# Optimization experiments

Hardware: AMD Instinct MI355X
Metric: run time of the kernel (lower is better)

## Reference

```python
import jax, jax.numpy as jnp
import numpy as np

B, S, D, F, E, K, R, H = 4, 1024, 1024, 512, 8, 2, 64, 256
TEMP = 1.0          # step=0 -> 0.5+0.5*cos(0)=1.0, clamp(min=0.1) -> 1.0
BW, EW, ZW = 0.3, 0.1, 1e-4


def fq(t):
    """Per-tensor symmetric int8 fake-quant with straight-through estimator."""
    s = jnp.maximum(jnp.max(jnp.abs(t)) / 127.0, 1e-8)
    q = jnp.clip(jnp.round(t / s), -128, 127) * s
    return t + jax.lax.stop_gradient(q - t)


def lora_lin(h, W, A, Bm):
    # base weight is frozen (requires_grad=False) and fake-quantized
    y = h @ fq(jax.lax.stop_gradient(W)).T + (h @ Bm.T) @ A.T
    return fq(y)


def ffn(h, w1, a1, b1, w2, a2, b2, w3, a3, b3):
    # use_swiglu=True path: gate = sigmoid(w3(x)); out = w2(w1(x)*gate); dropout=eval identity
    gate = jax.nn.sigmoid(lora_lin(h, w3, a3, b3))
    out = lora_lin(lora_lin(h, w1, a1, b1) * gate, w2, a2, b2)
    return fq(out)


def setup_inputs() -> dict:
    key = jax.random.key(0)
    k = jax.random.split(key, 32)
    n = lambda i, shp: jax.random.normal(k[i], shp, dtype=jnp.float32) * 0.02
    return {
        "x": jax.random.normal(k[0], (B, S, D), dtype=jnp.float32),
        "scorer_w": n(1, (E, D)), "scorer_b": jnp.zeros((E,), jnp.float32),
        "p1_w": n(2, (H, D)), "p1_b": jnp.zeros((H,), jnp.float32),
        "p2_w": n(3, (E, H)), "p2_b": jnp.zeros((E,), jnp.float32),
        "ew1_w": n(4, (E, F, D)), "ew1_a": n(5, (E, F, R)), "ew1_b": n(6, (E, R, D)),
        "ew2_w": n(7, (E, D, F)), "ew2_a": n(8, (E, D, R)), "ew2_b": n(9, (E, R, F)),
        "ew3_w": n(10, (E, F, D)), "ew3_a": n(11, (E, F, R)), "ew3_b": n(12, (E, R, D)),
        "s1_w": n(13, (F, D)), "s1_a": n(14, (F, R)), "s1_b": n(15, (R, D)),
        "s2_w": n(16, (D, F)), "s2_a": n(17, (D, R)), "s2_b": n(18, (R, F)),
        "s3_w": n(19, (F, D)), "s3_a": n(20, (F, R)), "s3_b": n(21, (R, D)),
    }


def reference(x, scorer_w, scorer_b, p1_w, p1_b, p2_w, p2_b,
              ew1_w, ew1_a, ew1_b, ew2_w, ew2_a, ew2_b, ew3_w, ew3_a, ew3_b,
              s1_w, s1_a, s1_b, s2_w, s2_a, s2_b, s3_w, s3_a, s3_b):
    xf = x.reshape(-1, D)                                           # [T, D]
    # --- router (per-token) ---
    base = (xf @ scorer_w.T + scorer_b) / TEMP                      # [T, E]
    policy = jax.nn.softmax(jax.nn.relu(xf @ p1_w.T + p1_b) @ p2_w.T + p2_b, axis=-1)
    scores = jax.nn.softmax((base + policy) * 0.5, axis=-1)         # fp32 softmax
    entropy = -(scores * jnp.log(scores + 1e-6)).sum(-1).mean()
    z_loss = ZW * (jax.nn.logsumexp(base, axis=-1) ** 2).mean()
    weights, indices = jax.lax.top_k(scores, K)                     # [T, K]
    weights = weights * TEMP
    cw = (jax.nn.one_hot(indices, E, dtype=weights.dtype) * weights[..., None]).sum(1)  # [T, E]
    usage = cw.sum(0)                                               # [E]
    uf = usage / (usage.mean() + 1e-6)
    balance_loss = BW * jnp.var(uf, ddof=1) - EW * entropy + z_loss
    # --- expert dispatch: dense masked combine (faithful to weighted scatter-add) ---
    eout = jax.vmap(lambda w1, a1, b1, w2, a2, b2, w3, a3, b3:
                    ffn(xf, w1, a1, b1, w2, a2, b2, w3, a3, b3))(
        ew1_w, ew1_a, ew1_b, ew2_w, ew2_a, ew2_b, ew3_w, ew3_a, ew3_b)  # [E, T, D]
    y = jnp.einsum('te,etd->td', cw, eout)                          # weighted combine
    z = ffn(xf, s1_w, s1_a, s1_b, s2_w, s2_a, s2_b, s3_w, s3_a, s3_b)
    out = (y + z).reshape(x.shape)
    return (out, usage, balance_loss, jnp.float32(0.0), jnp.float32(0.0))
```

## Files before the change

### kernel.cpp

```cpp
#include <hip/hip_runtime.h>

#define TTOK 4096
#define DDIM 1024
#define FDIM 512
#define NEXP 8
#define HDIM 256
#define RLORA 64
#define CROWS 14336

using u16 = unsigned short;
using f4v = __attribute__((ext_vector_type(4))) float;
using bfrag = __attribute__((ext_vector_type(8))) short;
using u16x8 = __attribute__((ext_vector_type(8))) unsigned short;

static __device__ __forceinline__ float bf2f(u16 u) {
  union { unsigned int u; float f; } x; x.u = ((unsigned int)u) << 16; return x.f;
}
static __device__ __forceinline__ u16 f2bf(float f) {
  union { float f; unsigned int u; } x; x.f = f;
  unsigned int r = (x.u + 0x7fffu + ((x.u >> 16) & 1u)) >> 16;
  return (u16)r;
}
static __device__ __forceinline__ float fq1(float t, float s) {
  float q = rintf(t / s);
  q = fminf(fmaxf(q, -128.f), 127.f);
  return q * s;
}

struct GemmGArgs {
  const u16* A; const u16* B; u16* C;
  const int* tokmap; const int2* blkmap; const int* nbrow;
};

#define STAGE1(d, kt, h, l) \
  __builtin_amdgcn_global_load_lds( \
    (const __attribute__((address_space(1))) void*)(gs[(h)*2+(l)] + (size_t)(kt)*64), \
    (__attribute__((address_space(3))) void*)&lds[(d)*32768 + (h)*8192 + (tid + (l)*512)*8], \
    16, 0, 0)

template <int MODE>
__global__ __launch_bounds__(512, 2) void gemm256g(GemmGArgs g) {
  const int br = blockIdx.x;
  if (br >= g.nbrow[0]) return;
  const int2 bm = g.blkmap[br];
  const int e = bm.x;
  const int m0 = bm.y;
  const int n0 = blockIdx.y * 256;
  const int tid = threadIdx.x;
  const int lane = tid & 63;
  const int wave = tid >> 6;
  const int wr = wave >> 2;
  const int wc = wave & 3;

  constexpr int K = MODE ? 1024 : 512;
  const u16* Bp = g.B + (size_t)e * (MODE ? 1048576 : 524288);

  __shared__ u16 lds[65536];

  const u16* gs[8];
#pragma unroll
  for (int h = 0; h < 4; h++)
#pragma unroll
    for (int l = 0; l < 2; l++) {
      const int slot = tid + l * 512;
      const int row = slot >> 3, p = slot & 7;
      const int glog = p ^ (row & 7);
      const u16* basep;
      if (h < 2) {
        const int grow = m0 + h * 128 + row;
        const int t = MODE ? g.tokmap[grow] : grow;
        basep = g.A + (size_t)t * K;
      } else {
        basep = Bp + (size_t)(n0 + (h - 2) * 128 + row) * K;
      }
      gs[h * 2 + l] = basep + glog * 8;
    }

  f4v acc[8][4];
#pragma unroll
  for (int i = 0; i < 8; i++)
#pragma unroll
    for (int j = 0; j < 4; j++) acc[i][j] = (f4v){0.f, 0.f, 0.f, 0.f};

  const int q = lane >> 4;
  const int lx = lane & 7;
  const int l15 = lane & 15;

#pragma unroll
  for (int h = 0; h < 4; h++) { STAGE1(0, 0, h, 0); STAGE1(0, 0, h, 1); }
  __syncthreads();

  constexpr int nt = K >> 6;
  for (int kt = 0; kt < nt; ++kt) {
    const int d = kt & 1;
    const int dn = d ^ 1;
    const bool more = (kt + 1 < nt);
#pragma unroll
    for (int kk = 0; kk < 2; ++kk) {
      if (more) {
        if (kk == 0) { STAGE1(dn, kt + 1, 0, 0); STAGE1(dn, kt + 1, 0, 1);
                       STAGE1(dn, kt + 1, 1, 0); STAGE1(dn, kt + 1, 1, 1); }
        else         { STAGE1(dn, kt + 1, 2, 0); STAGE1(dn, kt + 1, 2, 1);
                       STAGE1(dn, kt + 1, 3, 0); STAGE1(dn, kt + 1, 3, 1); }
      }
      bfrag afr[8], bfr[4];
      const int pa = ((kk * 4 + q) ^ lx) << 3;
      const int abase = d * 32768 + wr * 8192 + l15 * 64 + pa;
#pragma unroll
      for (int mi = 0; mi < 8; mi++) afr[mi] = *(const bfrag*)&lds[abase + mi * 1024];
      const int bbase = d * 32768 + (2 + (wc >> 1)) * 8192 + (((wc & 1) << 6) + l15) * 64 + pa;
#pragma unroll
      for (int ni = 0; ni < 4; ni++) bfr[ni] = *(const bfrag*)&lds[bbase + ni * 1024];
      __builtin_amdgcn_s_setprio(1);
#pragma unroll
      for (int mi = 0; mi < 8; mi++)
#pragma unroll
        for (int ni = 0; ni < 4; ni++)
          acc[mi][ni] = __builtin_amdgcn_mfma_f32_16x16x32_bf16(afr[mi], bfr[ni], acc[mi][ni], 0, 0, 0);
      __builtin_amdgcn_s_setprio(0);
    }
    __syncthreads();
  }

  const int crow0 = m0 + wr * 128 + q * 4;

  if (MODE == 1) {
    float* xlds = (float*)lds;
    const int lrow0 = wr * 128 + q * 4;
    if (wc >= 2) {
      const int lc = (wc - 2) * 64 + l15;
#pragma unroll
      for (int mi = 0; mi < 8; mi++)
#pragma unroll
        for (int ni = 0; ni < 4; ni++)
#pragma unroll
          for (int r = 0; r < 4; r++)
            xlds[(lrow0 + mi * 16 + r) * 128 + lc + ni * 16] = acc[mi][ni][r];
    }
    __syncthreads();
    if (wc < 2) {
      const int lc = wc * 64 + l15;
      const int fbase = (n0 >> 1) + lc;
#pragma unroll
      for (int mi = 0; mi < 8; mi++)
#pragma unroll
        for (int r = 0; r < 4; r++) {
          const int rowg = crow0 + mi * 16 + r;
          const int lr = lrow0 + mi * 16 + r;
#pragma unroll
          for (int ni = 0; ni < 4; ni++) {
            float y1 = acc[mi][ni][r];
            float y3 = xlds[lr * 128 + lc + ni * 16];
            float h = y1 / (1.f + __expf(-y3));
            g.C[(size_t)rowg * FDIM + fbase + ni * 16] = f2bf(h);
          }
        }
    }
  } else {
    const int ccol0 = n0 + wc * 64 + l15;
#pragma unroll
    for (int mi = 0; mi < 8; mi++)
#pragma unroll
      for (int ni = 0; ni < 4; ni++) {
        const int col = ccol0 + ni * 16;
#pragma unroll
        for (int r = 0; r < 4; r++)
          g.C[(size_t)(crow0 + mi * 16 + r) * 1024 + col] = f2bf(acc[mi][ni][r]);
      }
  }
}

struct FoldArgs {
  const u16* A0; const u16* B0;
  const u16* Wb;
  u16* C13; u16* C2e;
  const float* sW;
};

__global__ __launch_bounds__(256) void gemm_fold(FoldArgs g) {
  const int z = blockIdx.z;
  const bool is13 = z < 18;
  const int bx = blockIdx.x, by = blockIdx.y;
  if (is13 ? (bx >= 4) : (by >= 4)) return;
  const int N = is13 ? 1024 : 512;
  const int K = 64;
  const u16* Ap = is13 ? g.A0 + (size_t)z * 32768 : g.A0 + 589824 + (size_t)(z - 18) * 65536;
  const u16* Bp = is13 ? g.B0 + (size_t)z * 65536 : g.B0 + 1179648 + (size_t)(z - 18) * 32768;
  const u16* Wf = g.Wb + (size_t)z * 524288;
  u16* Cb; int flag;
  if (is13) {
    const int slot = (z >= 16) ? 8 : (z & 7);
    Cb = g.C13 + (size_t)slot * 1048576;
    flag = (z >= 8 && z < 16) || z == 17 ? 2 : 1;
  } else {
    Cb = g.C2e + (size_t)(z - 18) * 524288;
    flag = 0;
  }
  const float sw = fmaxf(g.sW[z] / 127.f, 1e-8f);

  const int tid = threadIdx.x;
  const int lane = tid & 63;
  const int wave = tid >> 6;
  const int wr = wave >> 1, wc = wave & 1;
  const int m0 = bx * 128, n0 = by * 128;

  __shared__ u16 As[128 * 32];
  __shared__ u16 Bs[128 * 32];
  __shared__ u16 stage[128 * 136];

  const int ldrow = tid >> 2;
  const int swzcol = (((tid & 3) ^ ((tid >> 3) & 3)) << 3);
  const u16* ga = Ap + (size_t)(m0 + ldrow) * K + swzcol;
  const u16* gb = Bp + (size_t)(n0 + ldrow) * K + swzcol;
  const size_t rowstep = (size_t)64 * K;

  f4v acc[4][4];
#pragma unroll
  for (int i = 0; i < 4; i++)
#pragma unroll
    for (int j = 0; j < 4; j++) acc[i][j] = (f4v){0.f, 0.f, 0.f, 0.f};

  const int rbase = lane & 15;
  const int q = lane >> 4;
  const int pg = (q ^ ((rbase >> 1) & 3)) << 3;
  const int arow = (wr << 6) + rbase;
  const int brow = (wc << 6) + rbase;

  for (int kt = 0; kt < K; kt += 32) {
    __builtin_amdgcn_global_load_lds((const __attribute__((address_space(1))) void*)(ga),
        (__attribute__((address_space(3))) void*)&As[tid * 8], 16, 0, 0);
    __builtin_amdgcn_global_load_lds((const __attribute__((address_space(1))) void*)(ga + rowstep),
        (__attribute__((address_space(3))) void*)&As[(256 + tid) * 8], 16, 0, 0);
    __builtin_amdgcn_global_load_lds((const __attribute__((address_space(1))) void*)(gb),
        (__attribute__((address_space(3))) void*)&Bs[tid * 8], 16, 0, 0);
    __builtin_amdgcn_global_load_lds((const __attribute__((address_space(1))) void*)(gb + rowstep),
        (__attribute__((address_space(3))) void*)&Bs[(256 + tid) * 8], 16, 0, 0);
    ga += 32; gb += 32;
    __syncthreads();
    bfrag af[4], bf[4];
#pragma unroll
    for (int mi = 0; mi < 4; mi++)
      af[mi] = *(const bfrag*)&As[(arow + mi * 16) * 32 + pg];
#pragma unroll
    for (int ni = 0; ni < 4; ni++)
      bf[ni] = *(const bfrag*)&Bs[(brow + ni * 16) * 32 + pg];
#pragma unroll
    for (int mi = 0; mi < 4; mi++)
#pragma unroll
      for (int ni = 0; ni < 4; ni++)
        acc[mi][ni] = __builtin_amdgcn_mfma_f32_16x16x32_bf16(af[mi], bf[ni], acc[mi][ni], 0, 0, 0);
    __syncthreads();
  }

  const int lrow0 = (wr << 6) + ((lane >> 4) << 2);
  const int lcol0 = (wc << 6) + (lane & 15);
#pragma unroll
  for (int mi = 0; mi < 4; mi++)
#pragma unroll
    for (int ni = 0; ni < 4; ni++) {
      const int n = lcol0 + ni * 16;
#pragma unroll
      for (int r = 0; r < 4; r++)
        stage[(lrow0 + mi * 16 + r) * 136 + n] = f2bf(acc[mi][ni][r]);
    }
  __syncthreads();

  const int dm0 = flag ? (((m0 >> 7) << 8) + (flag == 2 ? 128 : 0)) : m0;
#pragma unroll
  for (int j = 0; j < 8; j++) {
    const int s = j * 256 + tid;
    const int lr = s >> 4;
    const int n8 = (s & 15) << 3;
    const u16x8 wv = *(const u16x8*)&Wf[(size_t)(m0 + lr) * N + n0 + n8];
    const bfrag sv = *(const bfrag*)&stage[lr * 136 + n8];
    u16x8 o;
#pragma unroll
    for (int k = 0; k < 8; k++)
      o[k] = f2bf(fq1(bf2f(wv[k]), sw) + bf2f((u16)sv[k]));
    *(u16x8*)&Cb[(size_t)(dm0 + lr) * N + n0 + n8] = o;
  }
}

struct Gemm64Args { const u16* A; const u16* B; u16* Cb; int M, N, K; const float* bias; };
__global__ __launch_bounds__(256) void gemm64(Gemm64Args g) {
  const int tid = threadIdx.x;
  const int lane = tid & 63;
  const int wave = tid >> 6;
  const int wr = wave >> 1, wc = wave & 1;
  const int m0 = blockIdx.x * 64, n0 = blockIdx.y * 64;
  const int K = g.K, N = g.N;

  __shared__ u16 As[64 * 32];
  __shared__ u16 Bs[64 * 32];

  const int ldrow = tid >> 2;
  const int swzcol = (((tid & 3) ^ ((tid >> 3) & 3)) << 3);
  const u16* ga = g.A + (size_t)(m0 + ldrow) * K + swzcol;
  const u16* gb = g.B + (size_t)(n0 + ldrow) * K + swzcol;

  f4v acc[2][2];
#pragma unroll
  for (int i = 0; i < 2; i++)
#pragma unroll
    for (int j = 0; j < 2; j++) acc[i][j] = (f4v){0.f, 0.f, 0.f, 0.f};

  const int rbase = lane & 15;
  const int q = lane >> 4;
  const int pg = (q ^ ((rbase >> 1) & 3)) << 3;
  const int arow = (wr << 5) + rbase;
  const int brow = (wc << 5) + rbase;

  for (int kt = 0; kt < K; kt += 32) {
    __builtin_amdgcn_global_load_lds((const __attribute__((address_space(1))) void*)(ga),
        (__attribute__((address_space(3))) void*)&As[tid * 8], 16, 0, 0);
    __builtin_amdgcn_global_load_lds((const __attribute__((address_space(1))) void*)(gb),
        (__attribute__((address_space(3))) void*)&Bs[tid * 8], 16, 0, 0);
    ga += 32; gb += 32;
    __syncthreads();
    bfrag af[2], bf[2];
#pragma unroll
    for (int mi = 0; mi < 2; mi++)
      af[mi] = *(const bfrag*)&As[(arow + mi * 16) * 32 + pg];
#pragma unroll
    for (int ni = 0; ni < 2; ni++)
      bf[ni] = *(const bfrag*)&Bs[(brow + ni * 16) * 32 + pg];
#pragma unroll
    for (int mi = 0; mi < 2; mi++)
#pragma unroll
      for (int ni = 0; ni < 2; ni++)
        acc[mi][ni] = __builtin_amdgcn_mfma_f32_16x16x32_bf16(af[mi], bf[ni], acc[mi][ni], 0, 0, 0);
    __syncthreads();
  }

  const int crow0 = m0 + (wr << 5) + ((lane >> 4) << 2);
  const int ccol0 = n0 + (wc << 5) + (lane & 15);
#pragma unroll
  for (int mi = 0; mi < 2; mi++)
#pragma unroll
    for (int ni = 0; ni < 2; ni++) {
      const int n = ccol0 + ni * 16;
      const float b = g.bias[n];
#pragma unroll
      for (int r = 0; r < 4; r++) {
        float v = fmaxf(acc[mi][ni][r] + b, 0.f);
        g.Cb[(size_t)(crow0 + mi * 16 + r) * N + n] = f2bf(v);
      }
    }
}

struct AmaxCArgs { const float* W[27]; u16* Wraw; float* amax; };
__global__ __launch_bounds__(256) void amax_convw(AmaxCArgs a) {
  const int t = blockIdx.y;
  const float4* src = (const float4*)a.W[t];
  ushort4* dst = (ushort4*)(a.Wraw + (size_t)t * 524288);
  float lmax = 0.f;
  for (int i = blockIdx.x * 256 + threadIdx.x; i < 131072; i += gridDim.x * 256) {
    float4 v = src[i];
    ushort4 o; o.x = f2bf(v.x); o.y = f2bf(v.y); o.z = f2bf(v.z); o.w = f2bf(v.w);
    dst[i] = o;
    lmax = fmaxf(lmax, fmaxf(fmaxf(fabsf(v.x), fabsf(v.y)), fmaxf(fabsf(v.z), fabsf(v.w))));
  }
#pragma unroll
  for (int off = 32; off > 0; off >>= 1) lmax = fmaxf(lmax, __shfl_xor(lmax, off));
  __shared__ float wm[4];
  if ((threadIdx.x & 63) == 0) wm[threadIdx.x >> 6] = lmax;
  __syncthreads();
  if (threadIdx.x == 0) {
    float m = fmaxf(fmaxf(wm[0], wm[1]), fmaxf(wm[2], wm[3]));
    atomicMax((unsigned int*)&a.amax[t], __float_as_uint(m));
  }
}

struct ConvArgs {
  const float* xf; u16* xfb;
  const float* p1w; u16* p1wb;
  const float* Asrc[27]; u16* Adst;
  const float* Bsrc[27]; u16* Bdst;
};
__global__ __launch_bounds__(256) void convert_kernel(ConvArgs a) {
  const int g0 = blockIdx.x * 256 + threadIdx.x;
  const int stride = gridDim.x * 256;
  if (blockIdx.y == 0) {
    for (int i = g0; i < 1048576; i += stride) {
      float4 v = ((const float4*)a.xf)[i];
      ushort4 o; o.x = f2bf(v.x); o.y = f2bf(v.y); o.z = f2bf(v.z); o.w = f2bf(v.w);
      ((ushort4*)a.xfb)[i] = o;
    }
  } else if (blockIdx.y == 1) {
    for (int i = g0; i < 65536; i += stride) {
      float4 v = ((const float4*)a.p1w)[i];
      ushort4 o; o.x = f2bf(v.x); o.y = f2bf(v.y); o.z = f2bf(v.z); o.w = f2bf(v.w);
      ((ushort4*)a.p1wb)[i] = o;
    }
  } else if (blockIdx.y == 2) {
    for (int i = g0; i < 1179648; i += stride) {
      int t, off;
      if (i < 589824) { t = i >> 15; off = i & 32767; }
      else { int j = i - 589824; t = 18 + (j >> 16); off = j & 65535; }
      a.Adst[i] = f2bf(a.Asrc[t][off]);
    }
  } else {
    for (int i = g0; i < 1474560; i += stride) {
      int t, src;
      if (i < 1179648) { t = i >> 16; int off = i & 65535; src = (off & 63) * 1024 + (off >> 6); }
      else { int j = i - 1179648; t = 18 + (j >> 15); int off = j & 32767; src = (off & 63) * 512 + (off >> 6); }
      a.Bdst[i] = f2bf(a.Bsrc[t][src]);
    }
  }
}

struct RouterArgs {
  const float* xf; const u16* ph;
  const float* sw; const float* sb;
  const float* p2w; const float* p2b;
  float* base; float* pol;
};
__global__ __launch_bounds__(256) void router_small(RouterArgs a) {
  __shared__ float sw[8][1024];
  __shared__ float p2[8][256];
  const int tid = threadIdx.x;
  {
    const float4* s0 = (const float4*)a.sw;
    float4* d0 = (float4*)&sw[0][0];
    for (int i = tid; i < 2048; i += 256) d0[i] = s0[i];
    const float4* s1 = (const float4*)a.p2w;
    float4* d1 = (float4*)&p2[0][0];
    for (int i = tid; i < 512; i += 256) d1[i] = s1[i];
  }
  __syncthreads();
  const int tl = tid >> 4, s = tid & 15;
  const int token = blockIdx.x * 16 + tl;
  float acc[8] = {0,0,0,0,0,0,0,0}, pacc[8] = {0,0,0,0,0,0,0,0};
  const float4* xrow = (const float4*)(a.xf + (size_t)token * 1024);
  for (int i = 0; i < 16; i++) {
    const int d4 = i * 16 + s;
    float4 xv = xrow[d4];
#pragma unroll
    for (int e = 0; e < 8; e++) {
      float4 wv = ((const float4*)&sw[e][0])[d4];
      acc[e] += xv.x * wv.x + xv.y * wv.y + xv.z * wv.z + xv.w * wv.w;
    }
  }
  const u16* phrow = a.ph + (size_t)token * 256;
  for (int i = 0; i < 16; i++) {
    const int h = i * 16 + s;
    float pv = bf2f(phrow[h]);
#pragma unroll
    for (int e = 0; e < 8; e++) pacc[e] += pv * p2[e][h];
  }
#pragma unroll
  for (int off = 8; off > 0; off >>= 1)
#pragma unroll
    for (int e = 0; e < 8; e++) {
      acc[e] += __shfl_xor(acc[e], off);
      pacc[e] += __shfl_xor(pacc[e], off);
    }
  if (s == 0) {
#pragma unroll
    for (int e = 0; e < 8; e++) {
      a.base[token * 8 + e] = acc[e] + a.sb[e];
      a.pol[token * 8 + e] = pacc[e] + a.p2b[e];
    }
  }
}

struct FinArgs {
  const float* base; const float* pol;
  float* partials;
  int* idx2; float2* wb; int* cnt;
};
__global__ __launch_bounds__(256) void router_topk(FinArgs a) {
  const int tid = threadIdx.x;
  const int lane = tid & 63, wv = tid >> 6;
  const int token = blockIdx.x * 256 + tid;
  float b[8], p[8];
#pragma unroll
  for (int e = 0; e < 8; e++) { b[e] = a.base[token * 8 + e]; p[e] = a.pol[token * 8 + e]; }
  float pm = p[0];
#pragma unroll
  for (int e = 1; e < 8; e++) pm = fmaxf(pm, p[e]);
  float pe[8], psum = 0.f;
#pragma unroll
  for (int e = 0; e < 8; e++) { pe[e] = expf(p[e] - pm); psum += pe[e]; }
  const float pinv = 1.f / psum;
  float sl[8];
#pragma unroll
  for (int e = 0; e < 8; e++) sl[e] = (b[e] + pe[e] * pinv) * 0.5f;
  float sm = sl[0];
#pragma unroll
  for (int e = 1; e < 8; e++) sm = fmaxf(sm, sl[e]);
  float sc[8], ssum = 0.f;
#pragma unroll
  for (int e = 0; e < 8; e++) { sc[e] = expf(sl[e] - sm); ssum += sc[e]; }
  const float sinv = 1.f / ssum;
  float ent = 0.f;
#pragma unroll
  for (int e = 0; e < 8; e++) { float v = sc[e] * sinv; sc[e] = v; ent -= v * logf(v + 1e-6f); }
  float bm = b[0];
#pragma unroll
  for (int e = 1; e < 8; e++) bm = fmaxf(bm, b[e]);
  float zs = 0.f;
#pragma unroll
  for (int e = 0; e < 8; e++) zs += expf(b[e] - bm);
  const float lse = logf(zs) + bm;
  const float zt = lse * lse;
  float m1 = -1e30f, m2 = -1e30f; int i1 = 0, i2 = 0;
#pragma unroll
  for (int e = 0; e < 8; e++) {
    float v = sc[e];
    if (v > m1) { m2 = m1; i2 = i1; m1 = v; i1 = e; }
    else if (v > m2) { m2 = v; i2 = e; }
  }
  a.idx2[token] = i1 | (i2 << 8);
  a.wb[token] = make_float2(m1, m2);

  __shared__ int hist[8];
  if (tid < 8) hist[tid] = 0;
  __syncthreads();
  atomicAdd(&hist[i1], 1);
  atomicAdd(&hist[i2], 1);
  __syncthreads();
  if (tid < 8) atomicAdd(&a.cnt[tid], hist[tid]);

  float vals[10];
  vals[0] = ent; vals[1] = zt;
#pragma unroll
  for (int e = 0; e < 8; e++) vals[2 + e] = 0.f;
  vals[2 + i1] = m1; vals[2 + i2] = m2;
#pragma unroll
  for (int v = 0; v < 10; v++)
#pragma unroll
    for (int off = 32; off > 0; off >>= 1) vals[v] += __shfl_down(vals[v], off);
  __shared__ float wred[4][10];
  if (lane == 0)
#pragma unroll
    for (int v = 0; v < 10; v++) wred[wv][v] = vals[v];
  __syncthreads();
  if (tid < 10)
    a.partials[blockIdx.x * 10 + tid] = wred[0][tid] + wred[1][tid] + wred[2][tid] + wred[3][tid];
}

__global__ void setup_finalize(const int* cnt, int* off, int2* blkmap, int* nbrow, int* tokmap,
                               const float* partials, float* tail) {
  if (threadIdx.x == 0) {
    int o = 0, nb = 16;
    for (int i = 0; i < 16; i++) blkmap[i] = make_int2(8, i * 256);
    for (int e = 0; e < 8; e++) {
      off[e] = o;
      const int nbe = (cnt[e] + 255) >> 8;
      for (int i = 0; i < nbe; i++) blkmap[nb++] = make_int2(e, 4096 + o + i * 256);
      o += nbe << 8;
    }
    nbrow[0] = nb;
  } else if (threadIdx.x == 64) {
    float ent = 0.f, z = 0.f, us[8] = {0,0,0,0,0,0,0,0};
    for (int i = 0; i < 16; i++) {
      ent += partials[i * 10 + 0];
      z += partials[i * 10 + 1];
      for (int e = 0; e < 8; e++) us[e] += partials[i * 10 + 2 + e];
    }
    float tot = 0.f;
    for (int e = 0; e < 8; e++) tot += us[e];
    const float meanu = tot / 8.f;
    float uf[8], mu = 0.f;
    for (int e = 0; e < 8; e++) { uf[e] = us[e] / (meanu + 1e-6f); mu += uf[e]; }
    mu /= 8.f;
    float var = 0.f;
    for (int e = 0; e < 8; e++) { float d = uf[e] - mu; var += d * d; }
    var /= 7.f;
    const float bl = 0.3f * var - 0.1f * (ent / 4096.f) + 1e-4f * (z / 4096.f);
    for (int e = 0; e < 8; e++) tail[e] = us[e];
    tail[8] = bl; tail[9] = 0.f; tail[10] = 0.f;
  }
  for (int t = threadIdx.x; t < 4096; t += blockDim.x) tokmap[t] = t;
  for (int t = 4096 + threadIdx.x; t < CROWS; t += blockDim.x) tokmap[t] = 0;
}

__global__ __launch_bounds__(256) void compact_lists(const int* idx2, const int* off,
                                                     int* tokmap, int* posb) {
  const int e = blockIdx.x;
  const int tid = threadIdx.x;
  const int lane = tid & 63, wv = tid >> 6;
  __shared__ int wtot[4];
  __shared__ int carry;
  if (tid == 0) carry = 0;
  __syncthreads();
  const int base = 4096 + off[e];
  for (int c = 0; c < 16; c++) {
    const int t = c * 256 + tid;
    const int ii = idx2[t];
    const int i1 = ii & 255, i2 = ii >> 8;
    const int flag = (i1 == e || i2 == e) ? 1 : 0;
    const unsigned long long m = __ballot(flag);
    const int pre = __popcll(m & ((1ull << lane) - 1ull));
    if (lane == 63) wtot[wv] = pre + flag;
    __syncthreads();
    int wbase = 0;
    for (int i = 0; i < wv; i++) wbase += wtot[i];
    if (flag) {
      const int row = base + carry + wbase + pre;
      tokmap[row] = t;
      posb[t * 2 + (i2 == e ? 1 : 0)] = row;
    }
    __syncthreads();
    if (tid == 0) carry += wtot[0] + wtot[1] + wtot[2] + wtot[3];
    __syncthreads();
  }
}

__global__ __launch_bounds__(256) void combine_g(const u16* y2c, const int* posb,
                                                 const float2* wb, float* out) {
  const int t = blockIdx.x;
  const int c = threadIdx.x;
  const float2 w = wb[t];
  const int p1 = posb[t * 2], p2 = posb[t * 2 + 1];
  ushort4 s = ((const ushort4*)(y2c + (size_t)t * 1024))[c];
  ushort4 a = ((const ushort4*)(y2c + (size_t)p1 * 1024))[c];
  ushort4 b = ((const ushort4*)(y2c + (size_t)p2 * 1024))[c];
  float4 o;
  o.x = bf2f(s.x) + w.x * bf2f(a.x) + w.y * bf2f(b.x);
  o.y = bf2f(s.y) + w.x * bf2f(a.y) + w.y * bf2f(b.y);
  o.z = bf2f(s.z) + w.x * bf2f(a.z) + w.y * bf2f(b.z);
  o.w = bf2f(s.w) + w.x * bf2f(a.w) + w.y * bf2f(b.w);
  ((float4*)(out + (size_t)t * 1024))[c] = o;
}

extern "C" void kernel_launch(void* const* d_in, const int* in_sizes, int n_in,
                              void* d_out, int out_size, void* d_ws, size_t ws_size,
                              hipStream_t stream) {
  const float* x = (const float*)d_in[0];
  const float* scorer_w = (const float*)d_in[1];
  const float* scorer_b = (const float*)d_in[2];
  const float* p1_w = (const float*)d_in[3];
  const float* p1_b = (const float*)d_in[4];
  const float* p2_w = (const float*)d_in[5];
  const float* p2_b = (const float*)d_in[6];
  const float* ew1_w = (const float*)d_in[7];
  const float* ew1_a = (const float*)d_in[8];
  const float* ew1_b = (const float*)d_in[9];
  const float* ew2_w = (const float*)d_in[10];
  const float* ew2_a = (const float*)d_in[11];
  const float* ew2_b = (const float*)d_in[12];
  const float* ew3_w = (const float*)d_in[13];
  const float* ew3_a = (const float*)d_in[14];
  const float* ew3_b = (const float*)d_in[15];
  const float* s1_w = (const float*)d_in[16];
  const float* s1_a = (const float*)d_in[17];
  const float* s1_b = (const float*)d_in[18];
  const float* s2_w = (const float*)d_in[19];
  const float* s2_a = (const float*)d_in[20];
  const float* s2_b = (const float*)d_in[21];
  const float* s3_w = (const float*)d_in[22];
  const float* s3_a = (const float*)d_in[23];
  const float* s3_b = (const float*)d_in[24];
  float* outf = (float*)d_out;

  char* w = (char*)d_ws;
  auto alloc = [&](size_t bytes) { char* p = w; w += (bytes + 255) & ~(size_t)255; return p; };
  u16* xfb  = (u16*)alloc((size_t)TTOK * DDIM * 2);
  u16* ph   = (u16*)alloc((size_t)TTOK * HDIM * 2);
  u16* p1wb = (u16*)alloc((size_t)HDIM * DDIM * 2);
  u16* Adst = (u16*)alloc((size_t)1179648 * 2);
  u16* Bdst = (u16*)alloc((size_t)1474560 * 2);
  u16* Wraw = (u16*)alloc((size_t)27 * 524288 * 2);
  u16* W13  = (u16*)alloc((size_t)9 * 1024 * 1024 * 2);
  u16* W2e  = (u16*)alloc((size_t)9 * 1024 * 512 * 2);
  u16* h2c  = (u16*)alloc((size_t)CROWS * FDIM * 2);
  u16* y2c  = (u16*)alloc((size_t)CROWS * DDIM * 2);
  float* base = (float*)alloc((size_t)TTOK * 8 * 4);
  float* pol  = (float*)alloc((size_t)TTOK * 8 * 4);
  float* partials = (float*)alloc(16 * 10 * 4);
  float* amaxW = (float*)alloc(27 * 4);
  int* cnt    = (int*)alloc(8 * 4);
  int* off    = (int*)alloc(8 * 4);
  int2* blkmap = (int2*)alloc(64 * 8);
  int* nbrow  = (int*)alloc(4);
  int* tokmap = (int*)alloc(CROWS * 4);
  int* posb   = (int*)alloc(TTOK * 2 * 4);
  int* idx2   = (int*)alloc(TTOK * 4);
  float2* wb  = (float2*)alloc(TTOK * 8);

  hipMemsetAsync(amaxW, 0, 256 + 8 * 4, stream);

  {
    AmaxCArgs a{};
    for (int e = 0; e < 8; e++) {
      a.W[e] = ew1_w + (size_t)e * 524288;
      a.W[8 + e] = ew3_w + (size_t)e * 524288;
      a.W[18 + e] = ew2_w + (size_t)e * 524288;
    }
    a.W[16] = s1_w; a.W[17] = s3_w; a.W[26] = s2_w;
    a.Wraw = Wraw; a.amax = amaxW;
    hipLaunchKernelGGL(amax_convw, dim3(64, 27), dim3(256), 0, stream, a);
  }
  {
    ConvArgs c{};
    c.xf = x; c.xfb = xfb; c.p1w = p1_w; c.p1wb = p1wb;
    for (int e = 0; e < 8; e++) {
      c.Asrc[e] = ew1_a + (size_t)e * 32768;
      c.Asrc[8 + e] = ew3_a + (size_t)e * 32768;
      c.Asrc[18 + e] = ew2_a + (size_t)e * 65536;
      c.Bsrc[e] = ew1_b + (size_t)e * 65536;
      c.Bsrc[8 + e] = ew3_b + (size_t)e * 65536;
      c.Bsrc[18 + e] = ew2_b + (size_t)e * 32768;
    }
    c.Asrc[16] = s1_a; c.Asrc[17] = s3_a; c.Asrc[26] = s2_a;
    c.Bsrc[16] = s1_b; c.Bsrc[17] = s3_b; c.Bsrc[26] = s2_b;
    c.Adst = Adst; c.Bdst = Bdst;
    hipLaunchKernelGGL(convert_kernel, dim3(1024, 4), dim3(256), 0, stream, c);
  }
  {
    Gemm64Args g{};
    g.A = xfb; g.B = p1wb; g.Cb = ph;
    g.M = TTOK; g.N = HDIM; g.K = DDIM; g.bias = p1_b;
    hipLaunchKernelGGL(gemm64, dim3(64, 4), dim3(256), 0, stream, g);
  }
  {
    FoldArgs g{Adst, Bdst, Wraw, W13, W2e, amaxW};
    hipLaunchKernelGGL(gemm_fold, dim3(8, 8, 27), dim3(256), 0, stream, g);
  }
  {
    RouterArgs r{};
    r.xf = x; r.ph = ph; r.sw = scorer_w; r.sb = scorer_b;
    r.p2w = p2_w; r.p2b = p2_b; r.base = base; r.pol = pol;
    hipLaunchKernelGGL(router_small, dim3(256), dim3(256), 0, stream, r);
  }
  {
    FinArgs f{base, pol, partials, idx2, wb, cnt};
    hipLaunchKernelGGL(router_topk, dim3(16), dim3(256), 0, stream, f);
  }
  hipLaunchKernelGGL(setup_finalize, dim3(1), dim3(256), 0, stream,
                     cnt, off, blkmap, nbrow, tokmap, partials, outf + (size_t)TTOK * DDIM);
  hipLaunchKernelGGL(compact_lists, dim3(8), dim3(256), 0, stream, idx2, off, tokmap, posb);
  {
    GemmGArgs g{xfb, W13, h2c, tokmap, blkmap, nbrow};
    hipLaunchKernelGGL(gemm256g<1>, dim3(56, 4), dim3(512), 0, stream, g);
  }
  {
    GemmGArgs g{h2c, W2e, y2c, tokmap, blkmap, nbrow};
    hipLaunchKernelGGL(gemm256g<0>, dim3(56, 4), dim3(512), 0, stream, g);
  }
  hipLaunchKernelGGL(combine_g, dim3(4096), dim3(256), 0, stream, y2c, posb, wb, outf);
}
```

Before: 182.4 us.

## Merge prep kernels, read fp32 weights directly in fold, enlarge router GEMM tile

Folds the weight amax pass and the input/LoRA conversion into one prep kernel. The bf16 copy of the base weights is dropped, so gemm_fold reads the fp32 weights directly for fake-quant. The p1 router GEMM moves from 64x64 to 128x128 tiles, and setup_finalize is merged with compact_lists, with each block computing its own offsets. Together these cut launch count and the extra write and read of the weight copy, at the cost of fp32 weight reads in the fold epilogue and fewer blocks in the router GEMM.

```diff
diff --git a/kernel.cpp b/kernel.cpp
--- a/kernel.cpp
+++ b/kernel.cpp
@@ -172,7 +172,7 @@
 
 struct FoldArgs {
   const u16* A0; const u16* B0;
-  const u16* Wb;
+  const float* Wlist[27];
   u16* C13; u16* C2e;
   const float* sW;
 };
@@ -186,7 +186,7 @@
   const int K = 64;
   const u16* Ap = is13 ? g.A0 + (size_t)z * 32768 : g.A0 + 589824 + (size_t)(z - 18) * 65536;
   const u16* Bp = is13 ? g.B0 + (size_t)z * 65536 : g.B0 + 1179648 + (size_t)(z - 18) * 32768;
-  const u16* Wf = g.Wb + (size_t)z * 524288;
+  const float* Wf = g.Wlist[z];
   u16* Cb; int flag;
   if (is13) {
     const int slot = (z >= 16) ? 8 : (z & 7);
@@ -271,73 +271,80 @@
     const int s = j * 256 + tid;
     const int lr = s >> 4;
     const int n8 = (s & 15) << 3;
-    const u16x8 wv = *(const u16x8*)&Wf[(size_t)(m0 + lr) * N + n0 + n8];
+    const float4 w0 = *(const float4*)&Wf[(size_t)(m0 + lr) * N + n0 + n8];
+    const float4 w1 = *(const float4*)&Wf[(size_t)(m0 + lr) * N + n0 + n8 + 4];
     const bfrag sv = *(const bfrag*)&stage[lr * 136 + n8];
+    const float wa[8] = {w0.x, w0.y, w0.z, w0.w, w1.x, w1.y, w1.z, w1.w};
     u16x8 o;
 #pragma unroll
     for (int k = 0; k < 8; k++)
-      o[k] = f2bf(fq1(bf2f(wv[k]), sw) + bf2f((u16)sv[k]));
+      o[k] = f2bf(fq1(wa[k], sw) + bf2f((u16)sv[k]));
     *(u16x8*)&Cb[(size_t)(dm0 + lr) * N + n0 + n8] = o;
   }
 }
 
-struct Gemm64Args { const u16* A; const u16* B; u16* Cb; int M, N, K; const float* bias; };
-__global__ __launch_bounds__(256) void gemm64(Gemm64Args g) {
+struct Gemm128Args { const u16* A; const u16* B; u16* Cb; int N, K; const float* bias; };
+__global__ __launch_bounds__(256) void gemm128(Gemm128Args g) {
   const int tid = threadIdx.x;
   const int lane = tid & 63;
   const int wave = tid >> 6;
   const int wr = wave >> 1, wc = wave & 1;
-  const int m0 = blockIdx.x * 64, n0 = blockIdx.y * 64;
+  const int m0 = blockIdx.x * 128, n0 = blockIdx.y * 128;
   const int K = g.K, N = g.N;
 
-  __shared__ u16 As[64 * 32];
-  __shared__ u16 Bs[64 * 32];
+  __shared__ u16 As[128 * 32];
+  __shared__ u16 Bs[128 * 32];
 
   const int ldrow = tid >> 2;
   const int swzcol = (((tid & 3) ^ ((tid >> 3) & 3)) << 3);
   const u16* ga = g.A + (size_t)(m0 + ldrow) * K + swzcol;
   const u16* gb = g.B + (size_t)(n0 + ldrow) * K + swzcol;
-
-  f4v acc[2][2];
-#pragma unroll
-  for (int i = 0; i < 2; i++)
-#pragma unroll
-    for (int j = 0; j < 2; j++) acc[i][j] = (f4v){0.f, 0.f, 0.f, 0.f};
+  const size_t rowstep = (size_t)64 * K;
+
+  f4v acc[4][4];
+#pragma unroll
+  for (int i = 0; i < 4; i++)
+#pragma unroll
+    for (int j = 0; j < 4; j++) acc[i][j] = (f4v){0.f, 0.f, 0.f, 0.f};
 
   const int rbase = lane & 15;
   const int q = lane >> 4;
   const int pg = (q ^ ((rbase >> 1) & 3)) << 3;
-  const int arow = (wr << 5) + rbase;
-  const int brow = (wc << 5) + rbase;
+  const int arow = (wr << 6) + rbase;
+  const int brow = (wc << 6) + rbase;
 
   for (int kt = 0; kt < K; kt += 32) {
     __builtin_amdgcn_global_load_lds((const __attribute__((address_space(1))) void*)(ga),
         (__attribute__((address_space(3))) void*)&As[tid * 8], 16, 0, 0);
+    __builtin_amdgcn_global_load_lds((const __attribute__((address_space(1))) void*)(ga + rowstep),
+        (__attribute__((address_space(3))) void*)&As[(256 + tid) * 8], 16, 0, 0);
     __builtin_amdgcn_global_load_lds((const __attribute__((address_space(1))) void*)(gb),
         (__attribute__((address_space(3))) void*)&Bs[tid * 8], 16, 0, 0);
+    __builtin_amdgcn_global_load_lds((const __attribute__((address_space(1))) void*)(gb + rowstep),
+        (__attribute__((address_space(3))) void*)&Bs[(256 + tid) * 8], 16, 0, 0);
     ga += 32; gb += 32;
     __syncthreads();
-    bfrag af[2], bf[2];
-#pragma unroll
-    for (int mi = 0; mi < 2; mi++)
+    bfrag af[4], bf[4];
+#pragma unroll
+    for (int mi = 0; mi < 4; mi++)
       af[mi] = *(const bfrag*)&As[(arow + mi * 16) * 32 + pg];
 #pragma unroll
-    for (int ni = 0; ni < 2; ni++)
+    for (int ni = 0; ni < 4; ni++)
       bf[ni] = *(const bfrag*)&Bs[(brow + ni * 16) * 32 + pg];
 #pragma unroll
-    for (int mi = 0; mi < 2; mi++)
-#pragma unroll
-      for (int ni = 0; ni < 2; ni++)
+    for (int mi = 0; mi < 4; mi++)
+#pragma unroll
+      for (int ni = 0; ni < 4; ni++)
         acc[mi][ni] = __builtin_amdgcn_mfma_f32_16x16x32_bf16(af[mi], bf[ni], acc[mi][ni], 0, 0, 0);
     __syncthreads();
   }
 
-  const int crow0 = m0 + (wr << 5) + ((lane >> 4) << 2);
-  const int ccol0 = n0 + (wc << 5) + (lane & 15);
-#pragma unroll
-  for (int mi = 0; mi < 2; mi++)
-#pragma unroll
-    for (int ni = 0; ni < 2; ni++) {
+  const int crow0 = m0 + (wr << 6) + ((lane >> 4) << 2);
+  const int ccol0 = n0 + (wc << 6) + (lane & 15);
+#pragma unroll
+  for (int mi = 0; mi < 4; mi++)
+#pragma unroll
+    for (int ni = 0; ni < 4; ni++) {
       const int n = ccol0 + ni * 16;
       const float b = g.bias[n];
 #pragma unroll
@@ -348,51 +355,48 @@
     }
 }
 
-struct AmaxCArgs { const float* W[27]; u16* Wraw; float* amax; };
-__global__ __launch_bounds__(256) void amax_convw(AmaxCArgs a) {
-  const int t = blockIdx.y;
-  const float4* src = (const float4*)a.W[t];
-  ushort4* dst = (ushort4*)(a.Wraw + (size_t)t * 524288);
-  float lmax = 0.f;
-  for (int i = blockIdx.x * 256 + threadIdx.x; i < 131072; i += gridDim.x * 256) {
-    float4 v = src[i];
-    ushort4 o; o.x = f2bf(v.x); o.y = f2bf(v.y); o.z = f2bf(v.z); o.w = f2bf(v.w);
-    dst[i] = o;
-    lmax = fmaxf(lmax, fmaxf(fmaxf(fabsf(v.x), fabsf(v.y)), fmaxf(fabsf(v.z), fabsf(v.w))));
-  }
-#pragma unroll
-  for (int off = 32; off > 0; off >>= 1) lmax = fmaxf(lmax, __shfl_xor(lmax, off));
-  __shared__ float wm[4];
-  if ((threadIdx.x & 63) == 0) wm[threadIdx.x >> 6] = lmax;
-  __syncthreads();
-  if (threadIdx.x == 0) {
-    float m = fmaxf(fmaxf(wm[0], wm[1]), fmaxf(wm[2], wm[3]));
-    atomicMax((unsigned int*)&a.amax[t], __float_as_uint(m));
-  }
-}
-
-struct ConvArgs {
+struct PrepArgs {
+  const float* W[27]; float* amax;
   const float* xf; u16* xfb;
   const float* p1w; u16* p1wb;
   const float* Asrc[27]; u16* Adst;
   const float* Bsrc[27]; u16* Bdst;
 };
-__global__ __launch_bounds__(256) void convert_kernel(ConvArgs a) {
+__global__ __launch_bounds__(256) void prep_kernel(PrepArgs a) {
+  const int y = blockIdx.y;
   const int g0 = blockIdx.x * 256 + threadIdx.x;
   const int stride = gridDim.x * 256;
-  if (blockIdx.y == 0) {
-    for (int i = g0; i < 1048576; i += stride) {
-      float4 v = ((const float4*)a.xf)[i];
+  if (y < 27) {
+    const float4* src = (const float4*)a.W[y];
+    float lmax = 0.f;
+    for (int i = g0; i < 131072; i += stride) {
+      float4 v = src[i];
+      lmax = fmaxf(lmax, fmaxf(fmaxf(fabsf(v.x), fabsf(v.y)), fmaxf(fabsf(v.z), fabsf(v.w))));
+    }
+#pragma unroll
+    for (int off = 32; off > 0; off >>= 1) lmax = fmaxf(lmax, __shfl_xor(lmax, off));
+    __shared__ float wm[4];
+    if ((threadIdx.x & 63) == 0) wm[threadIdx.x >> 6] = lmax;
+    __syncthreads();
+    if (threadIdx.x == 0) {
+      float m = fmaxf(fmaxf(wm[0], wm[1]), fmaxf(wm[2], wm[3]));
+      atomicMax((unsigned int*)&a.amax[y], __float_as_uint(m));
+    }
+  } else if (y <= 30) {
+    const int qd = y - 27;
+    const float4* src = (const float4*)a.xf + (size_t)qd * 262144;
+    ushort4* dst = (ushort4*)a.xfb + (size_t)qd * 262144;
+    for (int i = g0; i < 262144; i += stride) {
+      float4 v = src[i];
       ushort4 o; o.x = f2bf(v.x); o.y = f2bf(v.y); o.z = f2bf(v.z); o.w = f2bf(v.w);
-      ((ushort4*)a.xfb)[i] = o;
-    }
-  } else if (blockIdx.y == 1) {
+      dst[i] = o;
+    }
+  } else if (y == 31) {
     for (int i = g0; i < 65536; i += stride) {
       float4 v = ((const float4*)a.p1w)[i];
       ushort4 o; o.x = f2bf(v.x); o.y = f2bf(v.y); o.z = f2bf(v.z); o.w = f2bf(v.w);
       ((ushort4*)a.p1wb)[i] = o;
     }
-  } else if (blockIdx.y == 2) {
     for (int i = g0; i < 1179648; i += stride) {
       int t, off;
       if (i < 589824) { t = i >> 15; off = i & 32767; }
@@ -540,52 +544,52 @@
     a.partials[blockIdx.x * 10 + tid] = wred[0][tid] + wred[1][tid] + wred[2][tid] + wred[3][tid];
 }
 
-__global__ void setup_finalize(const int* cnt, int* off, int2* blkmap, int* nbrow, int* tokmap,
-                               const float* partials, float* tail) {
-  if (threadIdx.x == 0) {
-    int o = 0, nb = 16;
-    for (int i = 0; i < 16; i++) blkmap[i] = make_int2(8, i * 256);
-    for (int e = 0; e < 8; e++) {
-      off[e] = o;
-      const int nbe = (cnt[e] + 255) >> 8;
-      for (int i = 0; i < nbe; i++) blkmap[nb++] = make_int2(e, 4096 + o + i * 256);
-      o += nbe << 8;
-    }
-    nbrow[0] = nb;
-  } else if (threadIdx.x == 64) {
-    float ent = 0.f, z = 0.f, us[8] = {0,0,0,0,0,0,0,0};
-    for (int i = 0; i < 16; i++) {
-      ent += partials[i * 10 + 0];
-      z += partials[i * 10 + 1];
-      for (int e = 0; e < 8; e++) us[e] += partials[i * 10 + 2 + e];
-    }
-    float tot = 0.f;
-    for (int e = 0; e < 8; e++) tot += us[e];
-    const float meanu = tot / 8.f;
-    float uf[8], mu = 0.f;
-    for (int e = 0; e < 8; e++) { uf[e] = us[e] / (meanu + 1e-6f); mu += uf[e]; }
-    mu /= 8.f;
-    float var = 0.f;
-    for (int e = 0; e < 8; e++) { float d = uf[e] - mu; var += d * d; }
-    var /= 7.f;
-    const float bl = 0.3f * var - 0.1f * (ent / 4096.f) + 1e-4f * (z / 4096.f);
-    for (int e = 0; e < 8; e++) tail[e] = us[e];
-    tail[8] = bl; tail[9] = 0.f; tail[10] = 0.f;
-  }
-  for (int t = threadIdx.x; t < 4096; t += blockDim.x) tokmap[t] = t;
-  for (int t = 4096 + threadIdx.x; t < CROWS; t += blockDim.x) tokmap[t] = 0;
-}
-
-__global__ __launch_bounds__(256) void compact_lists(const int* idx2, const int* off,
-                                                     int* tokmap, int* posb) {
+__global__ __launch_bounds__(256) void compact_setup(const int* idx2, const int* cnt,
+                                                     int2* blkmap, int* nbrow, int* tokmap,
+                                                     int* posb, const float* partials, float* tail) {
   const int e = blockIdx.x;
   const int tid = threadIdx.x;
+  if (e == 8) {
+    if (tid == 0) {
+      int o = 0, nb = 16;
+      for (int i = 0; i < 16; i++) blkmap[i] = make_int2(8, i * 256);
+      for (int ex = 0; ex < 8; ex++) {
+        const int nbe = (cnt[ex] + 255) >> 8;
+        for (int i = 0; i < nbe; i++) blkmap[nb++] = make_int2(ex, 4096 + o + i * 256);
+        o += nbe << 8;
+      }
+      nbrow[0] = nb;
+    } else if (tid == 64) {
+      float ent = 0.f, z = 0.f, us[8] = {0,0,0,0,0,0,0,0};
+      for (int i = 0; i < 16; i++) {
+        ent += partials[i * 10 + 0];
+        z += partials[i * 10 + 1];
+        for (int ex = 0; ex < 8; ex++) us[ex] += partials[i * 10 + 2 + ex];
+      }
+      float tot = 0.f;
+      for (int ex = 0; ex < 8; ex++) tot += us[ex];
+      const float meanu = tot / 8.f;
+      float uf[8], mu = 0.f;
+      for (int ex = 0; ex < 8; ex++) { uf[ex] = us[ex] / (meanu + 1e-6f); mu += uf[ex]; }
+      mu /= 8.f;
+      float var = 0.f;
+      for (int ex = 0; ex < 8; ex++) { float d = uf[ex] - mu; var += d * d; }
+      var /= 7.f;
+      const float bl = 0.3f * var - 0.1f * (ent / 4096.f) + 1e-4f * (z / 4096.f);
+      for (int ex = 0; ex < 8; ex++) tail[ex] = us[ex];
+      tail[8] = bl; tail[9] = 0.f; tail[10] = 0.f;
+    }
+    for (int t = tid; t < 4096; t += 256) tokmap[t] = t;
+    return;
+  }
   const int lane = tid & 63, wv = tid >> 6;
   __shared__ int wtot[4];
   __shared__ int carry;
   if (tid == 0) carry = 0;
   __syncthreads();
-  const int base = 4096 + off[e];
+  int off = 0;
+  for (int i = 0; i < e; i++) off += ((cnt[i] + 255) >> 8) << 8;
+  const int base = 4096 + off;
   for (int c = 0; c < 16; c++) {
     const int t = c * 256 + tid;
     const int ii = idx2[t];
@@ -606,6 +610,9 @@
     if (tid == 0) carry += wtot[0] + wtot[1] + wtot[2] + wtot[3];
     __syncthreads();
   }
+  const int ce = cnt[e];
+  const int pend = ((ce + 255) >> 8) << 8;
+  for (int r = ce + tid; r < pend; r += 256) tokmap[base + r] = 0;
 }
 
 __global__ __launch_bounds__(256) void combine_g(const u16* y2c, const int* posb,
@@ -662,7 +669,6 @@
   u16* p1wb = (u16*)alloc((size_t)HDIM * DDIM * 2);
   u16* Adst = (u16*)alloc((size_t)1179648 * 2);
   u16* Bdst = (u16*)alloc((size_t)1474560 * 2);
-  u16* Wraw = (u16*)alloc((size_t)27 * 524288 * 2);
   u16* W13  = (u16*)alloc((size_t)9 * 1024 * 1024 * 2);
   u16* W2e  = (u16*)alloc((size_t)9 * 1024 * 512 * 2);
   u16* h2c  = (u16*)alloc((size_t)CROWS * FDIM * 2);
@@ -672,7 +678,6 @@
   float* partials = (float*)alloc(16 * 10 * 4);
   float* amaxW = (float*)alloc(27 * 4);
   int* cnt    = (int*)alloc(8 * 4);
-  int* off    = (int*)alloc(8 * 4);
   int2* blkmap = (int2*)alloc(64 * 8);
   int* nbrow  = (int*)alloc(4);
   int* tokmap = (int*)alloc(CROWS * 4);
@@ -683,40 +688,39 @@
   hipMemsetAsync(amaxW, 0, 256 + 8 * 4, stream);
 
   {
-    AmaxCArgs a{};
+    PrepArgs a{};
     for (int e = 0; e < 8; e++) {
       a.W[e] = ew1_w + (size_t)e * 524288;
       a.W[8 + e] = ew3_w + (size_t)e * 524288;
       a.W[18 + e] = ew2_w + (size_t)e * 524288;
+      a.Asrc[e] = ew1_a + (size_t)e * 32768;
+      a.Asrc[8 + e] = ew3_a + (size_t)e * 32768;
+      a.Asrc[18 + e] = ew2_a + (size_t)e * 65536;
+      a.Bsrc[e] = ew1_b + (size_t)e * 65536;
+      a.Bsrc[8 + e] = ew3_b + (size_t)e * 65536;
+      a.Bsrc[18 + e] = ew2_b + (size_t)e * 32768;
     }
     a.W[16] = s1_w; a.W[17] = s3_w; a.W[26] = s2_w;
-    a.Wraw = Wraw; a.amax = amaxW;
-    hipLaunchKernelGGL(amax_convw, dim3(64, 27), dim3(256), 0, stream, a);
+    a.Asrc[16] = s1_a; a.Asrc[17] = s3_a; a.Asrc[26] = s2_a;
+    a.Bsrc[16] = s1_b; a.Bsrc[17] = s3_b; a.Bsrc[26] = s2_b;
+    a.amax = amaxW;
+    a.xf = x; a.xfb = xfb; a.p1w = p1_w; a.p1wb = p1wb;
+    a.Adst = Adst; a.Bdst = Bdst;
+    hipLaunchKernelGGL(prep_kernel, dim3(64, 33), dim3(256), 0, stream, a);
   }
   {
-    ConvArgs c{};
-    c.xf = x; c.xfb = xfb; c.p1w = p1_w; c.p1wb = p1wb;
+    Gemm128Args g{xfb, p1wb, ph, HDIM, DDIM, p1_b};
+    hipLaunchKernelGGL(gemm128, dim3(32, 2), dim3(256), 0, stream, g);
+  }
+  {
+    FoldArgs g{};
+    g.A0 = Adst; g.B0 = Bdst; g.C13 = W13; g.C2e = W2e; g.sW = amaxW;
     for (int e = 0; e < 8; e++) {
-      c.Asrc[e] = ew1_a + (size_t)e * 32768;
-      c.Asrc[8 + e] = ew3_a + (size_t)e * 32768;
-      c.Asrc[18 + e] = ew2_a + (size_t)e * 65536;
-      c.Bsrc[e] = ew1_b + (size_t)e * 65536;
-      c.Bsrc[8 + e] = ew3_b + (size_t)e * 65536;
-      c.Bsrc[18 + e] = ew2_b + (size_t)e * 32768;
-    }
-    c.Asrc[16] = s1_a; c.Asrc[17] = s3_a; c.Asrc[26] = s2_a;
-    c.Bsrc[16] = s1_b; c.Bsrc[17] = s3_b; c.Bsrc[26] = s2_b;
-    c.Adst = Adst; c.Bdst = Bdst;
-    hipLaunchKernelGGL(convert_kernel, dim3(1024, 4), dim3(256), 0, stream, c);
-  }
-  {
-    Gemm64Args g{};
-    g.A = xfb; g.B = p1wb; g.Cb = ph;
-    g.M = TTOK; g.N = HDIM; g.K = DDIM; g.bias = p1_b;
-    hipLaunchKernelGGL(gemm64, dim3(64, 4), dim3(256), 0, stream, g);
-  }
-  {
-    FoldArgs g{Adst, Bdst, Wraw, W13, W2e, amaxW};
+      g.Wlist[e] = ew1_w + (size_t)e * 524288;
+      g.Wlist[8 + e] = ew3_w + (size_t)e * 524288;
+      g.Wlist[18 + e] = ew2_w + (size_t)e * 524288;
+    }
+    g.Wlist[16] = s1_w; g.Wlist[17] = s3_w; g.Wlist[26] = s2_w;
     hipLaunchKernelGGL(gemm_fold, dim3(8, 8, 27), dim3(256), 0, stream, g);
   }
   {
@@ -729,9 +733,9 @@
     FinArgs f{base, pol, partials, idx2, wb, cnt};
     hipLaunchKernelGGL(router_topk, dim3(16), dim3(256), 0, stream, f);
   }
-  hipLaunchKernelGGL(setup_finalize, dim3(1), dim3(256), 0, stream,
-                     cnt, off, blkmap, nbrow, tokmap, partials, outf + (size_t)TTOK * DDIM);
-  hipLaunchKernelGGL(compact_lists, dim3(8), dim3(256), 0, stream, idx2, off, tokmap, posb);
+  hipLaunchKernelGGL(compact_setup, dim3(9), dim3(256), 0, stream,
+                     idx2, cnt, blkmap, nbrow, tokmap, posb, partials,
+                     outf + (size_t)TTOK * DDIM);
   {
     GemmGArgs g{xfb, W13, h2c, tokmap, blkmap, nbrow};
     hipLaunchKernelGGL(gemm256g<1>, dim3(56, 4), dim3(512), 0, stream, g);
```

Measured after the change: 225.7 us. +23.7%, slower.
